# Kernel tuning notes

Hardware: AMD Instinct MI355X
Metric: run time of the kernel (lower is better)

The kernel has to match this reference:

```python
import jax, jax.numpy as jnp
import numpy as np

BOX = 120          # box_size
RES = 1.0          # resolution (also Gaussian sigma)
NTYPES = 11        # num_atom_types (hard-coded in module)
D = 2              # splat half-width in cells -> (2D+1)^3 = 125 voxels/atom
B = 4
NATOMS = 2200      # 200 atoms per type


def setup_inputs() -> dict:
    key = jax.random.key(0)
    # atoms uniformly inside the box interior so splats mostly land in-bounds
    coords = jax.random.uniform(key, (B, NATOMS * 3), dtype=jnp.float32,
                                minval=20.0, maxval=100.0)
    per_type = NATOMS // NTYPES
    num_atoms_of_type = jnp.full((B, NTYPES), per_type, dtype=jnp.int32)
    offsets = jnp.tile(jnp.arange(NTYPES, dtype=jnp.int32) * per_type, (B, 1))
    return {"input_coords": coords,
            "num_atoms_of_type": num_atoms_of_type,
            "offsets": offsets}


def _splat(coords, num_atoms_of_type, offsets):
    # coords: [B, N, 3]; per-atom Gaussian splat into typed volume
    Bn, N, _ = coords.shape
    atom_idx = jnp.arange(N)

    def per_batch_types(off, num):
        # atoms [off[t], off[t]+num[t]) belong to type t
        t = jnp.clip(jnp.searchsorted(off, atom_idx, side='right') - 1, 0, NTYPES - 1)
        valid = (atom_idx >= off[t]) & (atom_idx < off[t] + num[t])
        return t, valid

    types, valid = jax.vmap(per_batch_types)(offsets, num_atoms_of_type)  # [B,N]

    # (2D+1)^3 window of integer cell offsets
    w = jnp.arange(-D, D + 1)
    wx, wy, wz = jnp.meshgrid(w, w, w, indexing='ij')
    win = jnp.stack([wx.ravel(), wy.ravel(), wz.ravel()], axis=-1)  # [W,3]

    base = jnp.floor(coords / RES).astype(jnp.int32)                 # [B,N,3]
    cells = base[:, :, None, :] + win[None, None, :, :]              # [B,N,W,3]
    centers = cells.astype(coords.dtype) * RES                       # voxel coords
    r2 = jnp.sum((centers - coords[:, :, None, :]) ** 2, axis=-1)    # [B,N,W]
    vals = jnp.exp(-r2 / (RES * RES))                                # Gaussian density

    inb = jnp.all((cells >= 0) & (cells < BOX), axis=-1)             # [B,N,W]
    ok = inb & valid[:, :, None]
    flat = (types[:, :, None] * (BOX * BOX * BOX)
            + cells[..., 0] * (BOX * BOX) + cells[..., 1] * BOX + cells[..., 2])
    flat = jnp.where(ok, flat, NTYPES * BOX * BOX * BOX)  # out-of-range -> dropped
    vals = jnp.where(ok, vals, jnp.zeros_like(vals))

    def scatter(f, v):
        vol = jnp.zeros((NTYPES * BOX * BOX * BOX,), dtype=coords.dtype)
        return vol.at[f.ravel()].add(v.ravel(), mode='drop')

    vol = jax.vmap(scatter)(flat, vals)
    return vol.reshape(Bn, NTYPES, BOX, BOX, BOX)


def reference(input_coords, num_atoms_of_type, offsets):
    coords = input_coords.reshape(input_coords.shape[0], -1, 3)
    return _splat(coords, num_atoms_of_type, offsets)
```

## Files before the change

kernel.cpp:

```cpp
#include <hip/hip_runtime.h>


#define BOX    120
#define NTYPES 11
#define DHALF  2
#define BOX3   (BOX * BOX * BOX)

#define BINSZ  4
#define NBIN   30
#define NBIN2  (NBIN * NBIN)
#define CAP    64

#define YT     8
#define NYT    (BOX / YT)
#define SCAP   512

__global__ void zero_counts_kernel(int* __restrict__ counts, int n) {
    int i = blockIdx.x * blockDim.x + threadIdx.x;
    if (i < n) counts[i] = 0;
}

__global__ void bin_kernel(const float* __restrict__ coords,
                           const int*  __restrict__ num_atoms_of_type,
                           const int*  __restrict__ offsets,
                           float4* __restrict__ bins,
                           int*    __restrict__ counts,
                           int batch, int natoms) {
    int gid = blockIdx.x * blockDim.x + threadIdx.x;
    if (gid >= batch * natoms) return;
    int b = gid / natoms;
    int i = gid - b * natoms;

    const float* c = coords + ((long long)b * natoms + i) * 3;
    float x = c[0], y = c[1], z = c[2];

    const int* off = offsets           + b * NTYPES;
    const int* num = num_atoms_of_type + b * NTYPES;

    int t = 0;
#pragma unroll
    for (int k = 1; k < NTYPES; ++k)
        if (off[k] <= i) t = k;
    if (!(i >= off[t] && i < off[t] + num[t])) return;

    int bx = (int)floorf(x);
    int by = (int)floorf(y);
    int bz = (int)floorf(z);
    if (bx < -DHALF || bx >= BOX + DHALF ||
        by < -DHALF || by >= BOX + DHALF ||
        bz < -DHALF || bz >= BOX + DHALF) return;

    int cbx = min(BOX - 1, max(0, bx)) / BINSZ;
    int cby = min(BOX - 1, max(0, by)) / BINSZ;
    int bin = b * NBIN2 + cbx * NBIN + cby;

    int slot = atomicAdd(&counts[bin], 1);
    if (slot < CAP)
        bins[(long long)bin * CAP + slot] =
            make_float4(x, y, z, __int_as_float(t));
}

__global__ __launch_bounds__(256)
void gather_kernel(const float4* __restrict__ bins,
                   const int*    __restrict__ counts,
                   float* __restrict__ out) {
    int bid = blockIdx.x;
    int yt = bid % NYT; bid /= NYT;
    int x  = bid % BOX; bid /= BOX;
    int b  = bid;
    int y0 = yt * YT;
    float xf = (float)x;

    __shared__ float4 raw[SCAP];
    __shared__ float4 srt[SCAP];
    __shared__ int cnt;
    __shared__ int tcnt[NTYPES];
    __shared__ int tstart[NTYPES + 1];
    __shared__ int tidx[NTYPES];

    if (threadIdx.x == 0) cnt = 0;
    if (threadIdx.x < NTYPES) tcnt[threadIdx.x] = 0;
    __syncthreads();

    int bxlo = max(0, x - DHALF) / BINSZ;
    int bxhi = min(BOX - 1, x + DHALF) / BINSZ;
    int bylo = max(0, y0 - DHALF) / BINSZ;
    int byhi = min(BOX - 1, y0 + YT - 1 + DHALF) / BINSZ;

    for (int cbx = bxlo; cbx <= bxhi; ++cbx) {
        for (int cby = bylo; cby <= byhi; ++cby) {
            int bin = b * NBIN2 + cbx * NBIN + cby;
            int c = min(counts[bin], CAP);
            const float4* lst = bins + (long long)bin * CAP;
            for (int j = threadIdx.x; j < c; j += blockDim.x) {
                float4 a = lst[j];
                float abx = floorf(a.x);
                float aby = floorf(a.y);
                if (fabsf(xf - abx) <= (float)DHALF &&
                    aby >= (float)(y0 - DHALF) &&
                    aby <= (float)(y0 + YT - 1 + DHALF)) {
                    int slot = atomicAdd(&cnt, 1);
                    if (slot < SCAP) {
                        int t = __float_as_int(a.w);
                        atomicAdd(&tcnt[t], 1);
                        float dx = xf - a.x;
                        raw[slot] = make_float4(a.y, a.z, dx * dx, a.w);
                    }
                }
            }
        }
    }
    __syncthreads();

    int n = min(cnt, SCAP);
    if (threadIdx.x == 0) {
        int s = 0;
#pragma unroll
        for (int k = 0; k < NTYPES; ++k) {
            tstart[k] = s; tidx[k] = s; s += tcnt[k];
        }
        tstart[NTYPES] = s;
    }
    __syncthreads();

    for (int j = threadIdx.x; j < n; j += blockDim.x) {
        float4 a = raw[j];
        int t = __float_as_int(a.w);
        int d = atomicAdd(&tidx[t], 1);
        srt[d] = a;
    }
    __syncthreads();

    int tt = threadIdx.x;
    int yl = tt / 30;
    int z4 = tt - yl * 30;
    bool on = (tt < 240);
    float yf  = (float)(y0 + yl);
    float zf0 = (float)(z4 * 4);

    float acc[NTYPES][4];
#pragma unroll
    for (int k = 0; k < NTYPES; ++k)
#pragma unroll
        for (int i = 0; i < 4; ++i) acc[k][i] = 0.f;

#pragma unroll
    for (int k = 0; k < NTYPES; ++k) {
        int s = tstart[k], e = tstart[k + 1];
        for (int j = s; j < e; ++j) {
            float4 a = srt[j];
            float ay = a.x, az = a.y, dx2 = a.z;
            float aby = floorf(ay);
            float abz = floorf(az);
            bool yok = fabsf(yf - aby) <= (float)DHALF;
            float dy  = yf - ay;
            float c2  = fmaf(dy, dy, dx2);
            float dz0  = zf0 - az;
            float dzc0 = zf0 - abz;
#pragma unroll
            for (int i = 0; i < 4; ++i) {
                float dz = dz0 + (float)i;
                float r2 = fmaf(dz, dz, c2);
                bool zok = fabsf(dzc0 + (float)i) <= (float)DHALF;
                float v = (yok && zok) ? expf(-r2) : 0.f;
                acc[k][i] += v;
            }
        }
    }

    if (on) {
        int base = x * (BOX * BOX) + (y0 + yl) * BOX + z4 * 4;
#pragma unroll
        for (int k = 0; k < NTYPES; ++k) {
            float4 v = make_float4(acc[k][0], acc[k][1], acc[k][2], acc[k][3]);
            *reinterpret_cast<float4*>(&out[(long long)(b * NTYPES + k) * BOX3 + base]) = v;
        }
    }
}

extern "C" void kernel_launch(void* const* d_in, const int* in_sizes, int n_in,
                              void* d_out, int out_size, void* d_ws, size_t ws_size,
                              hipStream_t stream) {
    const float* coords = (const float*)d_in[0];
    const int*   num    = (const int*)d_in[1];
    const int*   off    = (const int*)d_in[2];
    float*       out    = (float*)d_out;

    int batch  = in_sizes[1] / NTYPES;
    int natoms = in_sizes[0] / (3 * batch);

    int    nbins  = batch * NBIN2;
    int*   counts = (int*)d_ws;
    size_t bins_off = ((size_t)nbins * sizeof(int) + 15) & ~(size_t)15;
    float4* bins  = (float4*)((char*)d_ws + bins_off);

    zero_counts_kernel<<<(nbins + 255) / 256, 256, 0, stream>>>(counts, nbins);

    int natom_threads = batch * natoms;
    bin_kernel<<<(natom_threads + 255) / 256, 256, 0, stream>>>(
        coords, num, off, bins, counts, batch, natoms);

    gather_kernel<<<batch * BOX * NYT, 256, 0, stream>>>(bins, counts, out);
}
```

Measured before the change: 324.1 us.

## Replace per-voxel gather loop with per-atom LDS scatter into typed tile

The gather kernel no longer has every thread loop over all nearby atoms of every type and test each voxel. Instead, each block zeroes a shared-memory tile covering all types for its 8-row y slab. It then scatters the 5x5 y/z footprint of each candidate atom into that tile with LDS atomics, and the tile is streamed out with float4 stores. This removes the type-sorting pass and most wasted exp evaluations, and switches to the fast __expf. The costs are LDS atomic contention and a larger shared-memory footprint of about 42KB, which may lower occupancy. SCAP is also cut to 192, so atoms beyond that count in a block would be dropped.

```diff
diff --git a/kernel.cpp b/kernel.cpp
--- a/kernel.cpp
+++ b/kernel.cpp
@@ -13,7 +13,8 @@
 
 #define YT     8
 #define NYT    (BOX / YT)
-#define SCAP   512
+#define SCAP   192
+#define TILEF  (NTYPES * YT * BOX)
 
 __global__ void zero_counts_kernel(int* __restrict__ counts, int n) {
     int i = blockIdx.x * blockDim.x + threadIdx.x;
@@ -71,15 +72,14 @@
     int y0 = yt * YT;
     float xf = (float)x;
 
-    __shared__ float4 raw[SCAP];
+    __shared__ __align__(16) float tile[TILEF];
     __shared__ float4 srt[SCAP];
     __shared__ int cnt;
-    __shared__ int tcnt[NTYPES];
-    __shared__ int tstart[NTYPES + 1];
-    __shared__ int tidx[NTYPES];
 
+    float4* t4 = reinterpret_cast<float4*>(tile);
+    for (int i = threadIdx.x; i < TILEF / 4; i += 256)
+        t4[i] = make_float4(0.f, 0.f, 0.f, 0.f);
     if (threadIdx.x == 0) cnt = 0;
-    if (threadIdx.x < NTYPES) tcnt[threadIdx.x] = 0;
     __syncthreads();
 
     int bxlo = max(0, x - DHALF) / BINSZ;
@@ -92,7 +92,7 @@
             int bin = b * NBIN2 + cbx * NBIN + cby;
             int c = min(counts[bin], CAP);
             const float4* lst = bins + (long long)bin * CAP;
-            for (int j = threadIdx.x; j < c; j += blockDim.x) {
+            for (int j = threadIdx.x; j < c; j += 256) {
                 float4 a = lst[j];
                 float abx = floorf(a.x);
                 float aby = floorf(a.y);
@@ -101,80 +101,44 @@
                     aby <= (float)(y0 + YT - 1 + DHALF)) {
                     int slot = atomicAdd(&cnt, 1);
                     if (slot < SCAP) {
-                        int t = __float_as_int(a.w);
-                        atomicAdd(&tcnt[t], 1);
                         float dx = xf - a.x;
-                        raw[slot] = make_float4(a.y, a.z, dx * dx, a.w);
+                        srt[slot] = make_float4(a.y, a.z, dx * dx, a.w);
                     }
                 }
             }
         }
     }
     __syncthreads();
+    int n = min(cnt, SCAP);
 
-    int n = min(cnt, SCAP);
-    if (threadIdx.x == 0) {
-        int s = 0;
-#pragma unroll
-        for (int k = 0; k < NTYPES; ++k) {
-            tstart[k] = s; tidx[k] = s; s += tcnt[k];
-        }
-        tstart[NTYPES] = s;
+    for (int w = threadIdx.x; w < n * 25; w += 256) {
+        int j   = w / 25;
+        int rem = w - j * 25;
+        int iy  = rem / 5;
+        int iz  = rem - iy * 5;
+        float4 a = srt[j];
+        float ay = a.x, az = a.y, dx2 = a.z;
+        int t   = __float_as_int(a.w);
+        int aby = (int)floorf(ay);
+        int abz = (int)floorf(az);
+        int cy  = aby + iy - DHALF;
+        int cz  = abz + iz - DHALF;
+        if (cy < y0 || cy >= y0 + YT || (unsigned)cz >= (unsigned)BOX) continue;
+        float dy = (float)cy - ay;
+        float dz = (float)cz - az;
+        float r2 = fmaf(dy, dy, fmaf(dz, dz, dx2));
+        float v  = __expf(-r2);
+        atomicAdd(&tile[(t * YT + (cy - y0)) * BOX + cz], v);
     }
     __syncthreads();
 
-    for (int j = threadIdx.x; j < n; j += blockDim.x) {
-        float4 a = raw[j];
-        int t = __float_as_int(a.w);
-        int d = atomicAdd(&tidx[t], 1);
-        srt[d] = a;
-    }
-    __syncthreads();
-
-    int tt = threadIdx.x;
-    int yl = tt / 30;
-    int z4 = tt - yl * 30;
-    bool on = (tt < 240);
-    float yf  = (float)(y0 + yl);
-    float zf0 = (float)(z4 * 4);
-
-    float acc[NTYPES][4];
-#pragma unroll
-    for (int k = 0; k < NTYPES; ++k)
-#pragma unroll
-        for (int i = 0; i < 4; ++i) acc[k][i] = 0.f;
-
-#pragma unroll
-    for (int k = 0; k < NTYPES; ++k) {
-        int s = tstart[k], e = tstart[k + 1];
-        for (int j = s; j < e; ++j) {
-            float4 a = srt[j];
-            float ay = a.x, az = a.y, dx2 = a.z;
-            float aby = floorf(ay);
-            float abz = floorf(az);
-            bool yok = fabsf(yf - aby) <= (float)DHALF;
-            float dy  = yf - ay;
-            float c2  = fmaf(dy, dy, dx2);
-            float dz0  = zf0 - az;
-            float dzc0 = zf0 - abz;
-#pragma unroll
-            for (int i = 0; i < 4; ++i) {
-                float dz = dz0 + (float)i;
-                float r2 = fmaf(dz, dz, c2);
-                bool zok = fabsf(dzc0 + (float)i) <= (float)DHALF;
-                float v = (yok && zok) ? expf(-r2) : 0.f;
-                acc[k][i] += v;
-            }
-        }
-    }
-
-    if (on) {
-        int base = x * (BOX * BOX) + (y0 + yl) * BOX + z4 * 4;
-#pragma unroll
-        for (int k = 0; k < NTYPES; ++k) {
-            float4 v = make_float4(acc[k][0], acc[k][1], acc[k][2], acc[k][3]);
-            *reinterpret_cast<float4*>(&out[(long long)(b * NTYPES + k) * BOX3 + base]) = v;
-        }
+    long long obase = (long long)b * NTYPES * BOX3
+                    + (long long)x * (BOX * BOX) + (long long)y0 * BOX;
+    for (int i = threadIdx.x; i < NTYPES * 240; i += 256) {
+        int k = i / 240;
+        int r = i - k * 240;
+        float4 v = t4[k * 240 + r];
+        *reinterpret_cast<float4*>(&out[obase + (long long)k * BOX3 + r * 4]) = v;
     }
 }
 
```

After: 320.4 us. No clear change (-1.2%).
